# Kernel tuning notes

Hardware: AMD Instinct MI355X
Metric: run time of the kernel (lower is better)

## Reference

```python
import jax, jax.numpy as jnp
import numpy as np
from jax import lax

THRESHOLD = 0.5
KERNEL_SIZE = 4

# OpenCV morphologyEx(MORPH_OPEN) = erosion followed by dilation.
# For an even ksize k=4 with default anchor (-1,-1) -> anchor=(2,2):
#   erosion window offsets  = [-2, +1]  -> pad (2, 1)
#   dilation (kernel mirrored) offsets = [-1, +2] -> pad (1, 2)

def _erode(m, k):
    return lax.reduce_window(m, jnp.inf, lax.min,
                             window_dimensions=(1, k, k),
                             window_strides=(1, 1, 1),
                             padding=((0, 0), (k // 2, k - 1 - k // 2), (k // 2, k - 1 - k // 2)))

def _dilate(m, k):
    return lax.reduce_window(m, -jnp.inf, lax.max,
                             window_dimensions=(1, k, k),
                             window_strides=(1, 1, 1),
                             padding=((0, 0), (k - 1 - k // 2, k // 2), (k - 1 - k // 2, k // 2)))

def setup_inputs() -> dict:
    key = jax.random.key(0)
    k1, k2 = jax.random.split(key)
    score = jax.random.uniform(k1, (32, 1000), dtype=jnp.float32)
    mask = jax.random.uniform(k2, (32, 1024, 1024), dtype=jnp.float32)
    return {"score": score, "mask": mask}

def reference(score, mask):
    score = jnp.where(THRESHOLD <= score, score, jnp.zeros((), score.dtype))
    mask = jnp.where(THRESHOLD <= mask, mask, jnp.zeros((), mask.dtype))
    mask = _dilate(_erode(mask, KERNEL_SIZE), KERNEL_SIZE)  # morphological opening
    return (score, mask)
```

## Files before the change

kernel.cpp:

```cpp
#include <hip/hip_runtime.h>
#include <math.h>


#define H 1024
#define W 1024
#define R 16
#define STRIPS (H / R)
#define SEGS 4
#define BATCH 32
#define TASKS (STRIPS * SEGS * BATCH)
#define MASK_BLOCKS (TASKS / 4)
#define N_SCORE 32000
#define SCORE_BLOCKS ((N_SCORE + 255) / 256)
#define ITERS (R + 6)

__device__ __forceinline__ float th(float v) { return v >= 0.5f ? v : 0.0f; }

__global__ __launch_bounds__(256, 4)
void fused_kernel(const float* __restrict__ score,
                  const float* __restrict__ mask,
                  float* __restrict__ out) {
    const int bid0 = blockIdx.x;
    const int tid  = threadIdx.x;

    if (bid0 >= MASK_BLOCKS) {
        int i = (bid0 - MASK_BLOCKS) * 256 + tid;
        if (i < N_SCORE) out[i] = th(score[i]);
        return;
    }

    const int bid = (bid0 & 7) * (MASK_BLOCKS / 8) + (bid0 >> 3);

    const int wave = tid >> 6;
    const int lane = tid & 63;
    const int task = bid * 4 + wave;
    const int b    = task >> 8;
    const int rem  = task & 255;
    const int strip= rem >> 2;
    const int seg  = rem & 3;
    const int y0   = strip * R;
    const int c0   = seg * 256 + lane * 4;

    const float* img  = mask + (size_t)b * (H * W);
    float*       outp = out + N_SCORE + (size_t)b * (H * W);

    const bool eL = (c0 == 0);
    const bool eR = (c0 == W - 4);
    const int o0 = eL ? 0       : (c0 - 3);
    const int o1 = eR ? (W - 4) : (c0 + 1);
    const int o2 = eR ? (W - 2) : (c0 + 5);

    float4 B0[2], B1[2]; float2 B2[2];

#define ISSUE(IT2) do {                                                  \
        int t_  = y0 - 3 + (IT2);                                        \
        int tc_ = t_ < 0 ? 0 : (t_ >= H ? H - 1 : t_);      \
        const float* row_ = img + (size_t)tc_ * W;                       \
        __builtin_memcpy(&B0[(IT2) & 1], row_ + o0, 16);                 \
        __builtin_memcpy(&B1[(IT2) & 1], row_ + o1, 16);                 \
        __builtin_memcpy(&B2[(IT2) & 1], row_ + o2, 8);                  \
    } while (0)

    ISSUE(0);
    ISSUE(1);

    float hmP[7], q1[7], q2[7];
    #pragma unroll
    for (int m = 0; m < 7; ++m) { hmP[m] = q1[m] = q2[m] = INFINITY; }
    float hxP[4], u1[4], u2[4];
    #pragma unroll
    for (int j = 0; j < 4; ++j)  { hxP[j] = u1[j] = u2[j] = -INFINITY; }

    #pragma unroll
    for (int it = 0; it < ITERS; ++it) {
        const int t   = y0 - 3 + it;
        const int buf = it & 1;
        const bool rowOK = (t >= 0) && (t < H);

        float4 L0 = B0[buf], L1 = B1[buf]; float2 L2 = B2[buf];
        float ar[10];
        ar[0] = eL ? INFINITY : L0.x;
        ar[1] = eL ? INFINITY : L0.y;
        ar[2] = eL ? INFINITY : L0.z;
        ar[3] = eL ? L0.x     : L0.w;
        ar[4] = eR ? L1.y     : L1.x;
        ar[5] = eR ? L1.z     : L1.y;
        ar[6] = eR ? L1.w     : L1.z;
        ar[7] = eR ? INFINITY : L1.w;
        ar[8] = eR ? INFINITY : L2.x;
        ar[9] = eR ? INFINITY : L2.y;

        float p[9];
        #pragma unroll
        for (int m = 0; m < 9; ++m) p[m] = fminf(ar[m], ar[m + 1]);
        float hm[7];
        #pragma unroll
        for (int m = 0; m < 7; ++m) {
            float v = fminf(p[m], p[m + 2]);
            hm[m] = rowOK ? v : INFINITY;
        }

        if (it + 2 < ITERS) ISSUE(it + 2);

        const int r = t - 1;
        const float rlim = (r >= 0 && r < H) ? INFINITY : -INFINITY;
        float qt[7], ec[7];
        #pragma unroll
        for (int m = 0; m < 7; ++m) {
            qt[m] = fminf(hmP[m], hm[m]);
            ec[m] = fminf(fminf(qt[m], q2[m]), rlim);
        }
        ec[0] = eL ? -INFINITY : ec[0];
        ec[5] = eR ? -INFINITY : ec[5];
        ec[6] = eR ? -INFINITY : ec[6];

        #pragma unroll
        for (int m = 0; m < 7; ++m) { q2[m] = q1[m]; q1[m] = qt[m]; hmP[m] = hm[m]; }

        float p2[6];
        #pragma unroll
        for (int j = 0; j < 6; ++j) p2[j] = fmaxf(ec[j], ec[j + 1]);
        float hx[4], ur[4];
        #pragma unroll
        for (int j = 0; j < 4; ++j) {
            hx[j] = fmaxf(p2[j], p2[j + 2]);
            ur[j] = fmaxf(hxP[j], hx[j]);
        }

        if (it >= 6) {
            const int y = t - 3;
            float o[4];
            #pragma unroll
            for (int j = 0; j < 4; ++j)
                o[j] = th(fmaxf(ur[j], u2[j]));
            float* po = outp + (size_t)y * W + c0;
            *(float4*)(po) = make_float4(o[0], o[1], o[2], o[3]);
        }

        #pragma unroll
        for (int j = 0; j < 4; ++j) { u2[j] = u1[j]; u1[j] = ur[j]; hxP[j] = hx[j]; }
    }
#undef ISSUE
}

extern "C" void kernel_launch(void* const* d_in, const int* in_sizes, int n_in,
                              void* d_out, int out_size, void* d_ws, size_t ws_size,
                              hipStream_t stream) {
    const float* score = (const float*)d_in[0];
    const float* mask  = (const float*)d_in[1];
    float* out = (float*)d_out;

    const int grid = MASK_BLOCKS + SCORE_BLOCKS;
    fused_kernel<<<grid, 256, 0, stream>>>(score, mask, out);
}
```

Before: 263.5 us.

## Share horizontal halo via wave shuffles and triple-buffer row loads

```diff
diff --git a/kernel.cpp b/kernel.cpp
--- a/kernel.cpp
+++ b/kernel.cpp
@@ -16,20 +16,22 @@
 
 __device__ __forceinline__ float th(float v) { return v >= 0.5f ? v : 0.0f; }
 
-__global__ __launch_bounds__(256, 4)
+__global__ __launch_bounds__(256)
+__attribute__((amdgpu_waves_per_eu(4, 4)))
 void fused_kernel(const float* __restrict__ score,
                   const float* __restrict__ mask,
                   float* __restrict__ out) {
     const int bid0 = blockIdx.x;
     const int tid  = threadIdx.x;
 
-    if (bid0 >= MASK_BLOCKS) {
-        int i = (bid0 - MASK_BLOCKS) * 256 + tid;
+    if (bid0 < SCORE_BLOCKS) {
+        int i = bid0 * 256 + tid;
         if (i < N_SCORE) out[i] = th(score[i]);
         return;
     }
+    const int mb0 = bid0 - SCORE_BLOCKS;
 
-    const int bid = (bid0 & 7) * (MASK_BLOCKS / 8) + (bid0 >> 3);
+    const int bid = (mb0 & 7) * (MASK_BLOCKS / 8) + (mb0 >> 3);
 
     const int wave = tid >> 6;
     const int lane = tid & 63;
@@ -46,23 +48,21 @@
 
     const bool eL = (c0 == 0);
     const bool eR = (c0 == W - 4);
-    const int o0 = eL ? 0       : (c0 - 3);
-    const int o1 = eR ? (W - 4) : (c0 + 1);
-    const int o2 = eR ? (W - 2) : (c0 + 5);
+    const bool sm = (lane == 0) || (lane == 63);
+    const int oS = (lane == 0) ? (eL ? 0 : c0 - 4)
+                               : (eR ? W - 4 : c0 + 4);
 
-    float4 B0[2], B1[2]; float2 B2[2];
+    float4 own[3], seam[3];
 
-#define ISSUE(IT2) do {                                                  \
-        int t_  = y0 - 3 + (IT2);                                        \
+#define ISSUE(IT) do {                                                   \
+        int t_  = y0 - 3 + (IT);                                         \
         int tc_ = t_ < 0 ? 0 : (t_ >= H ? H - 1 : t_);      \
         const float* row_ = img + (size_t)tc_ * W;                       \
-        __builtin_memcpy(&B0[(IT2) & 1], row_ + o0, 16);                 \
-        __builtin_memcpy(&B1[(IT2) & 1], row_ + o1, 16);                 \
-        __builtin_memcpy(&B2[(IT2) & 1], row_ + o2, 8);                  \
+        own[(IT) % 3] = *(const float4*)(row_ + c0);                     \
+        if (sm) seam[(IT) % 3] = *(const float4*)(row_ + oS);            \
     } while (0)
 
-    ISSUE(0);
-    ISSUE(1);
+    ISSUE(0); ISSUE(1); ISSUE(2);
 
     float hmP[7], q1[7], q2[7];
     #pragma unroll
@@ -74,21 +74,33 @@
     #pragma unroll
     for (int it = 0; it < ITERS; ++it) {
         const int t   = y0 - 3 + it;
-        const int buf = it & 1;
+        const int buf = it % 3;
         const bool rowOK = (t >= 0) && (t < H);
 
-        float4 L0 = B0[buf], L1 = B1[buf]; float2 L2 = B2[buf];
+        float4 ow = own[buf];
+        float4 sw = seam[buf];
+        float a0 = __shfl_up(ow.y, 1);
+        float a1 = __shfl_up(ow.z, 1);
+        float a2 = __shfl_up(ow.w, 1);
+        float a7 = __shfl_down(ow.x, 1);
+        float a8 = __shfl_down(ow.y, 1);
+        float a9 = __shfl_down(ow.z, 1);
+        a0 = (lane == 0)  ? sw.y : a0;
+        a1 = (lane == 0)  ? sw.z : a1;
+        a2 = (lane == 0)  ? sw.w : a2;
+        a7 = (lane == 63) ? sw.x : a7;
+        a8 = (lane == 63) ? sw.y : a8;
+        a9 = (lane == 63) ? sw.z : a9;
         float ar[10];
-        ar[0] = eL ? INFINITY : L0.x;
-        ar[1] = eL ? INFINITY : L0.y;
-        ar[2] = eL ? INFINITY : L0.z;
-        ar[3] = eL ? L0.x     : L0.w;
-        ar[4] = eR ? L1.y     : L1.x;
-        ar[5] = eR ? L1.z     : L1.y;
-        ar[6] = eR ? L1.w     : L1.z;
-        ar[7] = eR ? INFINITY : L1.w;
-        ar[8] = eR ? INFINITY : L2.x;
-        ar[9] = eR ? INFINITY : L2.y;
+        ar[0] = eL ? INFINITY : a0;
+        ar[1] = eL ? INFINITY : a1;
+        ar[2] = eL ? INFINITY : a2;
+        ar[3] = ow.x;  ar[4] = ow.y;  ar[5] = ow.z;  ar[6] = ow.w;
+        ar[7] = eR ? INFINITY : a7;
+        ar[8] = eR ? INFINITY : a8;
+        ar[9] = eR ? INFINITY : a9;
+
+        if (it + 3 < ITERS) ISSUE(it + 3);
 
         float p[9];
         #pragma unroll
@@ -99,8 +111,6 @@
             float v = fminf(p[m], p[m + 2]);
             hm[m] = rowOK ? v : INFINITY;
         }
-
-        if (it + 2 < ITERS) ISSUE(it + 2);
 
         const int r = t - 1;
         const float rlim = (r >= 0 && r < H) ? INFINITY : -INFINITY;
```

After: 265.1 us. No clear change (+0.6%).
